# Kernel tuning notes

Measured on AMD Instinct MI355X. Metric: run time of the kernel, lower is better.

Reference implementation:

```python
import jax, jax.numpy as jnp
from jax import lax
import numpy as np

H = 16  # GRU hidden = 4**N_GRAM * 4
V = 4   # 4**N_GRAM
B = 512
S = 8192


def _gru_cell(x, h, Wih, Whh, bih, bhh):
    # PyTorch GRU gate ordering: r, z, n
    gi = x @ Wih.T + bih          # [B, 3H]
    gh = h @ Whh.T + bhh          # [B, 3H]
    ir, iz, inn = jnp.split(gi, 3, axis=-1)
    hr, hz, hn = jnp.split(gh, 3, axis=-1)
    r = jax.nn.sigmoid(ir + hr)
    z = jax.nn.sigmoid(iz + hz)
    n = jnp.tanh(inn + r * hn)
    return (1.0 - z) * n + z * h


def setup_inputs() -> dict:
    key = jax.random.key(0)
    ks = jax.random.split(key, 12)
    f32 = jnp.float32
    k_i = 1.0 / np.sqrt(H)  # torch default GRU/Linear init scale
    u = lambda k, shp: jax.random.uniform(k, shp, f32, -k_i, k_i)
    gt = jax.random.normal(ks[0], (B, V, S), f32)
    return {
        "ground_truth": gt,
        "enc_Wih": u(ks[1], (3 * H, V)),
        "enc_Whh": u(ks[2], (3 * H, H)),
        "enc_bih": u(ks[3], (3 * H,)),
        "enc_bhh": u(ks[4], (3 * H,)),
        "dec_Wih": u(ks[5], (3 * H, V)),
        "dec_Whh": u(ks[6], (3 * H, H)),
        "dec_bih": u(ks[7], (3 * H,)),
        "dec_bhh": u(ks[8], (3 * H,)),
        "out_W": u(ks[9], (V, H)),
        "out_b": u(ks[10], (V,)),
        "emb": jnp.eye(V, dtype=f32),  # one-hot Embedding_LUT (frozen)
        "tf_rate": 1,
    }


def reference(ground_truth, enc_Wih, enc_Whh, enc_bih, enc_bhh,
              dec_Wih, dec_Whh, dec_bih, dec_bhh, out_W, out_b, emb, tf_rate):
    gt = jnp.transpose(ground_truth, (2, 0, 1))      # [S, B, V]
    seq_l, batch, _ = gt.shape
    dt = gt.dtype
    h0 = jnp.zeros((batch, H), dt)

    def enc_step(h, x):
        return _gru_cell(x, h, enc_Wih, enc_Whh, enc_bih, enc_bhh), None
    enc_hidden, _ = lax.scan(enc_step, h0, gt)

    targets = jnp.argmax(gt, axis=2)                 # [S, B] int
    x0 = jnp.zeros((batch, V), dt)
    loss0 = jnp.asarray(0.0, dt)

    if tf_rate >= 1:  # argmax-feedback branch (random() < tf_rate always true)
        def dec_step(carry, tgt):
            x, h, loss = carry
            h = _gru_cell(x, h, dec_Wih, dec_Whh, dec_bih, dec_bhh)
            out = h @ out_W.T + out_b                # [B, V]
            logp = jax.nn.log_softmax(out, axis=-1)
            nll = -jnp.mean(jnp.take_along_axis(logp, tgt[:, None], axis=1))
            top_i = jnp.argmax(out, axis=-1)
            return (emb[top_i], h, loss + nll), None
        (_, _, loss), _ = lax.scan(dec_step, (x0, enc_hidden, loss0), targets)
        output_batch = jnp.zeros((seq_l, batch, V), dt)  # never written in this branch
    else:  # teacher-forcing branch (NLLLoss applied to raw logits, as in source)
        def dec_step(carry, inp):
            x, h, loss = carry
            gt_t, tgt = inp
            h = _gru_cell(x, h, dec_Wih, dec_Whh, dec_bih, dec_bhh)
            out = h @ out_W.T + out_b
            nll = -jnp.mean(jnp.take_along_axis(out, tgt[:, None], axis=1))
            return (gt_t, h, loss + nll), out
        (_, _, loss), output_batch = lax.scan(dec_step, (x0, enc_hidden, loss0), (gt, targets))

    return loss, jnp.transpose(output_batch, (1, 2, 0))  # [B, V, S]
```

## Files before the change

### kernel.cpp

```cpp
#include <hip/hip_runtime.h>

#define S_LEN 8192
#define NH 16
#define NV 4
#define NB 512

typedef _Float16 h2 __attribute__((ext_vector_type(2)));

#define L2E  1.4426950408889634f
#define L2E2 2.8853900817779268f

template<int R>
__device__ __forceinline__ float rotf(float v) {
    return __int_as_float(__builtin_amdgcn_mov_dpp(__float_as_int(v), 0x120 + R, 0xF, 0xF, true));
}
template<int R>
__device__ __forceinline__ h2 roth(h2 v) {
    int i;
    __builtin_memcpy(&i, &v, 4);
    i = __builtin_amdgcn_mov_dpp(i, 0x120 + R, 0xF, 0xF, true);
    h2 o;
    __builtin_memcpy(&o, &i, 4);
    return o;
}
__device__ __forceinline__ float qxor1(float v) {
    return __int_as_float(__builtin_amdgcn_mov_dpp(__float_as_int(v), 0xB1, 0xF, 0xF, true));
}
__device__ __forceinline__ float qxor2(float v) {
    return __int_as_float(__builtin_amdgcn_mov_dpp(__float_as_int(v), 0x4E, 0xF, 0xF, true));
}
__device__ __forceinline__ float qxor3(float v) {
    return __int_as_float(__builtin_amdgcn_mov_dpp(__float_as_int(v), 0x1B, 0xF, 0xF, true));
}

__device__ __forceinline__ float fex2(float x) { return __builtin_amdgcn_exp2f(x); }
__device__ __forceinline__ float frcp(float x) { return __builtin_amdgcn_rcpf(x); }
__device__ __forceinline__ float fsig2(float x) { return frcp(1.0f + fex2(-x)); }
__device__ __forceinline__ float4 ld4(const float* p) { return *(const float4*)p; }

__device__ __forceinline__ h2 pkh(float a, float b) {
    auto t = __builtin_amdgcn_cvt_pkrtz(a, b);
    h2 o;
    __builtin_memcpy(&o, &t, 4);
    return o;
}

__device__ __forceinline__ void bcast32(float v, float& lo, float& hi) {
    lo = v;
    asm("v_permlane32_swap_b32 %0, %1" : "+v"(lo), "+v"(v));
    hi = v;
}

#define FILL_HP16(hp, h)                                      \
    do {                                                      \
        h2 p0_ = pkh((h), rotf<1>(h));                        \
        hp[0] = p0_;                                          \
        hp[1] = roth<2>(p0_);                                 \
        hp[2] = roth<4>(p0_);                                 \
        hp[3] = roth<6>(p0_);                                 \
        hp[4] = roth<8>(p0_);                                 \
        hp[5] = roth<10>(p0_);                                \
        hp[6] = roth<12>(p0_);                                \
        hp[7] = roth<14>(p0_);                                \
    } while (0)

__device__ __forceinline__ float dotd2(const h2* __restrict__ w, const h2* hp, float start) {
    float a = __builtin_amdgcn_fdot2(w[0], hp[0], start, false);
    float b = __builtin_amdgcn_fdot2(w[1], hp[1], 0.0f, false);
    a = __builtin_amdgcn_fdot2(w[2], hp[2], a, false);
    b = __builtin_amdgcn_fdot2(w[3], hp[3], b, false);
    a = __builtin_amdgcn_fdot2(w[4], hp[4], a, false);
    b = __builtin_amdgcn_fdot2(w[5], hp[5], b, false);
    a = __builtin_amdgcn_fdot2(w[6], hp[6], a, false);
    b = __builtin_amdgcn_fdot2(w[7], hp[7], b, false);
    return a + b;
}
__device__ __forceinline__ float dotd2x(const h2* __restrict__ w, const h2* hp, float start) {
    float a = __builtin_amdgcn_fdot2(w[0], hp[0], start, false);
    float b = __builtin_amdgcn_fdot2(w[1], hp[1], 0.0f, false);
    a = __builtin_amdgcn_fdot2(w[2], hp[2], a, false);
    b = __builtin_amdgcn_fdot2(w[3], hp[3], b, false);
    a = __builtin_amdgcn_fdot2(w[4], hp[4], a, false);
    b = __builtin_amdgcn_fdot2(w[5], hp[5], b, false);
    a = __builtin_amdgcn_fdot2(w[6], hp[6], a, false);
    b = __builtin_amdgcn_fdot2(w[7], hp[7], b, false);
    a = __builtin_amdgcn_fdot2(w[8], hp[8], a, false);
    b = __builtin_amdgcn_fdot2(w[9], hp[9], b, false);
    return a + b;
}

__global__ __launch_bounds__(64, 1) void rnn_kernel(
    const float* __restrict__ gt,
    const float* __restrict__ eWih, const float* __restrict__ eWhh,
    const float* __restrict__ ebih, const float* __restrict__ ebhh,
    const float* __restrict__ dWih, const float* __restrict__ dWhh,
    const float* __restrict__ dbih, const float* __restrict__ dbhh,
    const float* __restrict__ oW,  const float* __restrict__ ob,
    float* __restrict__ outs)
{
    const int lane = threadIdx.x;
    const int j    = lane & 15;
    const int q    = j & 3;
    const int row  = lane >> 4;
    const bool isLo = (lane < 32);
    const int b    = blockIdx.x * 2 + (row & 1);

    int probe = __builtin_amdgcn_mov_dpp(j, 0x121, 0xF, 0xF, true);
    const int sgn = (probe == ((j + 1) & 15)) ? 1 : -1;

    float h = 0.0f;

    {
        const float* gb = gt + (size_t)b * (NV * S_LEN);
        const int gA = isLo ? 0 : 1;
        h2 wA[10], wB[10];
#pragma unroll
        for (int p = 0; p < 8; ++p) {
            int k0 = (j + sgn * (2 * p)) & 15;
            int k1 = (j + sgn * (2 * p + 1)) & 15;
            wA[p] = (h2){(_Float16)(L2E * eWhh[(gA * NH + j) * NH + k0]),
                         (_Float16)(L2E * eWhh[(gA * NH + j) * NH + k1])};
            float n0 = isLo ? (L2E2 * eWhh[(2 * NH + j) * NH + k0]) : 0.0f;
            float n1 = isLo ? (L2E2 * eWhh[(2 * NH + j) * NH + k1]) : 0.0f;
            wB[p] = (h2){(_Float16)n0, (_Float16)n1};
        }
#pragma unroll
        for (int p = 0; p < 2; ++p) {
            wA[8 + p] = (h2){(_Float16)(L2E * eWih[(gA * NH + j) * NV + 2 * p]),
                             (_Float16)(L2E * eWih[(gA * NH + j) * NV + 2 * p + 1])};
            float n0 = isLo ? 0.0f : (L2E2 * eWih[(2 * NH + j) * NV + 2 * p]);
            float n1 = isLo ? 0.0f : (L2E2 * eWih[(2 * NH + j) * NV + 2 * p + 1]);
            wB[8 + p] = (h2){(_Float16)n0, (_Float16)n1};
        }
        const float startA = L2E * (ebih[gA * NH + j] + ebhh[gA * NH + j]);
        const float startB = isLo ? (L2E2 * ebhh[2 * NH + j]) : (L2E2 * ebih[2 * NH + j]);

        auto estep = [&](float x0, float x1, float x2, float x3) {
            h2 hp[10];
            FILL_HP16(hp, h);
            hp[8] = pkh(x0, x1);
            hp[9] = pkh(x2, x3);
            float vA = dotd2x(wA, hp, startA);
            float vB = dotd2x(wB, hp, startB);
            float ar, az, hn, inn;
            bcast32(vA, ar, az);
            bcast32(vB, hn, inn);
            float r  = fsig2(ar);
            float z  = fsig2(az);
            float y  = fmaf(r, hn, inn);
            float w2 = fsig2(y);
            float t2 = fmaf(-2.0f, z, 2.0f);
            float tb = fmaf(z, h, z - 1.0f);
            h = fmaf(w2, t2, tb);
        };

        float4 A0 = ld4(gb + 0 * S_LEN), A1 = ld4(gb + 1 * S_LEN),
               A2 = ld4(gb + 2 * S_LEN), A3 = ld4(gb + 3 * S_LEN);
        float4 B0 = ld4(gb + 0 * S_LEN + 4), B1 = ld4(gb + 1 * S_LEN + 4),
               B2 = ld4(gb + 2 * S_LEN + 4), B3 = ld4(gb + 3 * S_LEN + 4);
        for (int t = 0; t < S_LEN; t += 8) {
            estep(A0.x, A1.x, A2.x, A3.x);
            estep(A0.y, A1.y, A2.y, A3.y);
            estep(A0.z, A1.z, A2.z, A3.z);
            estep(A0.w, A1.w, A2.w, A3.w);
            int ta = t + 8;  if (ta > S_LEN - 4) ta = S_LEN - 4;
            A0 = ld4(gb + 0 * S_LEN + ta); A1 = ld4(gb + 1 * S_LEN + ta);
            A2 = ld4(gb + 2 * S_LEN + ta); A3 = ld4(gb + 3 * S_LEN + ta);
            estep(B0.x, B1.x, B2.x, B3.x);
            estep(B0.y, B1.y, B2.y, B3.y);
            estep(B0.z, B1.z, B2.z, B3.z);
            estep(B0.w, B1.w, B2.w, B3.w);
            int tb2 = t + 12; if (tb2 > S_LEN - 4) tb2 = S_LEN - 4;
            B0 = ld4(gb + 0 * S_LEN + tb2); B1 = ld4(gb + 1 * S_LEN + tb2);
            B2 = ld4(gb + 2 * S_LEN + tb2); B3 = ld4(gb + 3 * S_LEN + tb2);
        }
    }

    const int gA = isLo ? 0 : 1;
    h2 wA[8], wB[8];
#pragma unroll
    for (int p = 0; p < 8; ++p) {
        int k0 = (j + sgn * (2 * p)) & 15;
        int k1 = (j + sgn * (2 * p + 1)) & 15;
        wA[p] = (h2){(_Float16)(L2E * dWhh[(gA * NH + j) * NH + k0]),
                     (_Float16)(L2E * dWhh[(gA * NH + j) * NH + k1])};
        float w0 = isLo ? (L2E2 * dWhh[(2 * NH + j) * NH + k0]) : oW[q * NH + k0];
        float w1 = isLo ? (L2E2 * dWhh[(2 * NH + j) * NH + k1]) : oW[q * NH + k1];
        wB[p] = (h2){(_Float16)w0, (_Float16)w1};
    }
    const float bNi  = dbih[2 * NH + j];
    const float bNiS = L2E2 * bNi;
    const float biasA  = L2E * (dbih[gA * NH + j] + dbhh[gA * NH + j]);
    const float startB = isLo ? (L2E2 * dbhh[2 * NH + j]) : ob[q];
    float SA[NV], KN[NV];
#pragma unroll
    for (int m = 0; m < NV; ++m) {
        int c = m ^ q;
        SA[m] = L2E * dWih[(gA * NH + j) * NV + c];
        KN[m] = L2E2 * (bNi + dWih[(2 * NH + j) * NV + c]);
    }

    int oidx = (b << 15) + q;
    const bool storer = isLo && (j < 4);

    auto dstep = [&](int koff) {
        h2 hp[8];
        FILL_HP16(hp, h);
        float aA = dotd2(wA, hp, biasA);
        float vB = dotd2(wB, hp, startB);
        float hn, oa;
        bcast32(vB, hn, oa);
        if (storer) outs[oidx + koff] = oa;
        float ob_ = qxor1(oa);
        float oc_ = qxor2(oa);
        float od_ = qxor3(oa);
        bool cA = ob_ > oa;  float mA = fmaxf(oa, ob_);
        bool cB = od_ > oc_; float mB = fmaxf(oc_, od_);
        bool hi_ = mB > mA;
        float KA  = hi_ ? (cB ? SA[3] : SA[2]) : (cA ? SA[1] : SA[0]);
        float KN_ = hi_ ? (cB ? KN[3] : KN[2]) : (cA ? KN[1] : KN[0]);
        float sg  = fsig2(aA + KA);
        float r, z;
        bcast32(sg, r, z);
        float y   = fmaf(r, hn, KN_);
        float w2  = fsig2(y);
        float t2  = fmaf(-2.0f, z, 2.0f);
        float tb  = fmaf(z, h, z - 1.0f);
        h = fmaf(w2, t2, tb);
    };

    {
        h2 hp[8];
        FILL_HP16(hp, h);
        float aA = dotd2(wA, hp, biasA);
        float vB = dotd2(wB, hp, startB);
        float hn, oa;
        bcast32(vB, hn, oa);
        float sg = fsig2(aA);
        float r, z;
        bcast32(sg, r, z);
        float y  = fmaf(r, hn, bNiS);
        float w2 = fsig2(y);
        float t2 = fmaf(-2.0f, z, 2.0f);
        float tb = fmaf(z, h, z - 1.0f);
        h = fmaf(w2, t2, tb);
    }
    for (int u = 0; u < 8184; u += 8) {
#pragma unroll
        for (int k = 0; k < 8; ++k) dstep(k * 4);
        oidx += 32;
    }
#pragma unroll
    for (int k = 0; k < 7; ++k) dstep(k * 4);
    oidx += 28;

    {
        h2 hp[8];
        FILL_HP16(hp, h);
        float vB = dotd2(wB, hp, startB);
        float hn, oa;
        bcast32(vB, hn, oa);
        if (storer) outs[oidx] = oa;
    }
}

__global__ __launch_bounds__(1024) void loss_kernel(
    const float* __restrict__ gt, float* __restrict__ outs, float* __restrict__ loss)
{
    int tid = blockIdx.x * 1024 + threadIdx.x;
    int t = tid & (S_LEN - 1);
    int b = tid >> 13;
    float4 o = *(const float4*)(outs + (size_t)tid * 4);
    const float* g = gt + (size_t)b * (NV * S_LEN) + t;
    float p0 = g[0], p1 = g[S_LEN], p2 = g[2 * S_LEN], p3 = g[3 * S_LEN];
    int tg = (p1 > p0) ? 1 : 0;  float bm = fmaxf(p0, p1);
    tg = (p2 > bm) ? 2 : tg;     bm = fmaxf(p2, bm);
    tg = (p3 > bm) ? 3 : tg;
    float vt = (tg & 1) ? ((tg & 2) ? o.w : o.y) : ((tg & 2) ? o.z : o.x);
    float mx = fmaxf(fmaxf(o.x, o.y), fmaxf(o.z, o.w));
    float ss = __expf(o.x - mx) + __expf(o.y - mx) + __expf(o.z - mx) + __expf(o.w - mx);
    float v  = (mx - vt) + __logf(ss);
    *(float4*)(outs + (size_t)tid * 4) = make_float4(0.f, 0.f, 0.f, 0.f);
#pragma unroll
    for (int d = 1; d < 64; d <<= 1) v += __shfl_xor(v, d, 64);
    __shared__ float sm[16];
    int w = threadIdx.x >> 6;
    if ((threadIdx.x & 63) == 0) sm[w] = v;
    __syncthreads();
    if (threadIdx.x < 16) {
        float s = sm[threadIdx.x];
#pragma unroll
        for (int d = 1; d < 16; d <<= 1) s += __shfl_xor(s, d, 64);
        if (threadIdx.x == 0) atomicAdd(loss, s * (1.0f / NB));
    }
}

extern "C" void kernel_launch(void* const* d_in, const int* in_sizes, int n_in,
                              void* d_out, int out_size, void* d_ws, size_t ws_size,
                              hipStream_t stream) {
    (void)in_sizes; (void)n_in; (void)d_ws; (void)ws_size; (void)out_size;
    const float* gt   = (const float*)d_in[0];
    const float* eWih = (const float*)d_in[1];
    const float* eWhh = (const float*)d_in[2];
    const float* ebih = (const float*)d_in[3];
    const float* ebhh = (const float*)d_in[4];
    const float* dWih = (const float*)d_in[5];
    const float* dWhh = (const float*)d_in[6];
    const float* dbih = (const float*)d_in[7];
    const float* dbhh = (const float*)d_in[8];
    const float* oW   = (const float*)d_in[9];
    const float* ob   = (const float*)d_in[10];

    float* out  = (float*)d_out;
    float* outs = out + 1;
    (void)hipMemsetAsync(d_out, 0, sizeof(float), stream);
    rnn_kernel<<<NB / 2, 64, 0, stream>>>(gt, eWih, eWhh, ebih, ebhh,
                                          dWih, dWhh, dbih, dbhh, oW, ob, outs);
    loss_kernel<<<(NB * S_LEN) / 1024, 1024, 0, stream>>>(gt, outs, out);
}
```

Baseline: 2.987 ms.

## Assign one batch row per wave, spreading gate rows across 64 lanes

Result: faster. 2.875 ms (median of 2 runs) (-3.7%).

```diff
diff --git a/kernel.cpp b/kernel.cpp
--- a/kernel.cpp
+++ b/kernel.cpp
@@ -49,6 +49,11 @@
     lo = v;
     asm("v_permlane32_swap_b32 %0, %1" : "+v"(lo), "+v"(v));
     hi = v;
+}
+__device__ __forceinline__ void bcast16(float v, float& e, float& o) {
+    e = v;
+    asm("v_permlane16_swap_b32 %0, %1" : "+v"(e), "+v"(v));
+    o = v;
 }
 
 #define FILL_HP16(hp, h)                                      \
@@ -64,29 +69,17 @@
         hp[7] = roth<14>(p0_);                                \
     } while (0)
 
-__device__ __forceinline__ float dotd2(const h2* __restrict__ w, const h2* hp, float start) {
-    float a = __builtin_amdgcn_fdot2(w[0], hp[0], start, false);
-    float b = __builtin_amdgcn_fdot2(w[1], hp[1], 0.0f, false);
-    a = __builtin_amdgcn_fdot2(w[2], hp[2], a, false);
-    b = __builtin_amdgcn_fdot2(w[3], hp[3], b, false);
-    a = __builtin_amdgcn_fdot2(w[4], hp[4], a, false);
-    b = __builtin_amdgcn_fdot2(w[5], hp[5], b, false);
-    a = __builtin_amdgcn_fdot2(w[6], hp[6], a, false);
-    b = __builtin_amdgcn_fdot2(w[7], hp[7], b, false);
-    return a + b;
-}
-__device__ __forceinline__ float dotd2x(const h2* __restrict__ w, const h2* hp, float start) {
-    float a = __builtin_amdgcn_fdot2(w[0], hp[0], start, false);
-    float b = __builtin_amdgcn_fdot2(w[1], hp[1], 0.0f, false);
-    a = __builtin_amdgcn_fdot2(w[2], hp[2], a, false);
-    b = __builtin_amdgcn_fdot2(w[3], hp[3], b, false);
-    a = __builtin_amdgcn_fdot2(w[4], hp[4], a, false);
-    b = __builtin_amdgcn_fdot2(w[5], hp[5], b, false);
-    a = __builtin_amdgcn_fdot2(w[6], hp[6], a, false);
-    b = __builtin_amdgcn_fdot2(w[7], hp[7], b, false);
-    a = __builtin_amdgcn_fdot2(w[8], hp[8], a, false);
-    b = __builtin_amdgcn_fdot2(w[9], hp[9], b, false);
-    return a + b;
+__device__ __forceinline__ float dot8s(const h2* __restrict__ w, const h2* hp, float start) {
+    float a = start;
+#pragma unroll
+    for (int p = 0; p < 8; ++p) a = __builtin_amdgcn_fdot2(w[p], hp[p], a, false);
+    return a;
+}
+__device__ __forceinline__ float dot10s(const h2* __restrict__ w, const h2* hp, float start) {
+    float a = start;
+#pragma unroll
+    for (int p = 0; p < 10; ++p) a = __builtin_amdgcn_fdot2(w[p], hp[p], a, false);
+    return a;
 }
 
 __global__ __launch_bounds__(64, 1) void rnn_kernel(
@@ -102,8 +95,8 @@
     const int j    = lane & 15;
     const int q    = j & 3;
     const int row  = lane >> 4;
-    const bool isLo = (lane < 32);
-    const int b    = blockIdx.x * 2 + (row & 1);
+    const bool loH = (lane < 32);
+    const int b    = blockIdx.x;
 
     int probe = __builtin_amdgcn_mov_dpp(j, 0x121, 0xF, 0xF, true);
     const int sgn = (probe == ((j + 1) & 15)) ? 1 : -1;
@@ -112,42 +105,44 @@
 
     {
         const float* gb = gt + (size_t)b * (NV * S_LEN);
-        const int gA = isLo ? 0 : 1;
-        h2 wA[10], wB[10];
-#pragma unroll
-        for (int p = 0; p < 8; ++p) {
-            int k0 = (j + sgn * (2 * p)) & 15;
-            int k1 = (j + sgn * (2 * p + 1)) & 15;
-            wA[p] = (h2){(_Float16)(L2E * eWhh[(gA * NH + j) * NH + k0]),
-                         (_Float16)(L2E * eWhh[(gA * NH + j) * NH + k1])};
-            float n0 = isLo ? (L2E2 * eWhh[(2 * NH + j) * NH + k0]) : 0.0f;
-            float n1 = isLo ? (L2E2 * eWhh[(2 * NH + j) * NH + k1]) : 0.0f;
-            wB[p] = (h2){(_Float16)n0, (_Float16)n1};
+        h2 w[10];
+        float start;
+        {
+            const int g  = (row == 0) ? 0 : (row == 2) ? 1 : 2;
+            const float schh = (row == 0 || row == 2) ? L2E : (row == 1 ? L2E2 : 0.0f);
+            const float scih = (row == 0 || row == 2) ? L2E : (row == 3 ? L2E2 : 0.0f);
+#pragma unroll
+            for (int p = 0; p < 8; ++p) {
+                int k0 = (j + sgn * (2 * p)) & 15;
+                int k1 = (j + sgn * (2 * p + 1)) & 15;
+                w[p] = (h2){(_Float16)(schh * eWhh[(g * NH + j) * NH + k0]),
+                            (_Float16)(schh * eWhh[(g * NH + j) * NH + k1])};
+            }
+#pragma unroll
+            for (int p = 0; p < 2; ++p) {
+                w[8 + p] = (h2){(_Float16)(scih * eWih[(g * NH + j) * NV + 2 * p]),
+                                (_Float16)(scih * eWih[(g * NH + j) * NV + 2 * p + 1])};
+            }
+            start = (row == 0) ? L2E  * (ebih[j] + ebhh[j])
+                  : (row == 2) ? L2E  * (ebih[NH + j] + ebhh[NH + j])
+                  : (row == 1) ? L2E2 * ebhh[2 * NH + j]
+                               : L2E2 * ebih[2 * NH + j];
         }
-#pragma unroll
-        for (int p = 0; p < 2; ++p) {
-            wA[8 + p] = (h2){(_Float16)(L2E * eWih[(gA * NH + j) * NV + 2 * p]),
-                             (_Float16)(L2E * eWih[(gA * NH + j) * NV + 2 * p + 1])};
-            float n0 = isLo ? 0.0f : (L2E2 * eWih[(2 * NH + j) * NV + 2 * p]);
-            float n1 = isLo ? 0.0f : (L2E2 * eWih[(2 * NH + j) * NV + 2 * p + 1]);
-            wB[8 + p] = (h2){(_Float16)n0, (_Float16)n1};
-        }
-        const float startA = L2E * (ebih[gA * NH + j] + ebhh[gA * NH + j]);
-        const float startB = isLo ? (L2E2 * ebhh[2 * NH + j]) : (L2E2 * ebih[2 * NH + j]);
 
         auto estep = [&](float x0, float x1, float x2, float x3) {
             h2 hp[10];
             FILL_HP16(hp, h);
             hp[8] = pkh(x0, x1);
             hp[9] = pkh(x2, x3);
-            float vA = dotd2x(wA, hp, startA);
-            float vB = dotd2x(wB, hp, startB);
-            float ar, az, hn, inn;
-            bcast32(vA, ar, az);
-            bcast32(vB, hn, inn);
-            float r  = fsig2(ar);
-            float z  = fsig2(az);
-            float y  = fmaf(r, hn, inn);
+            float v = dot10s(w, hp, start);
+            float e, o_;
+            bcast16(v, e, o_);
+            float hn_, inn_;
+            bcast32(o_, hn_, inn_);
+            float sg = fsig2(e);
+            float r, z;
+            bcast32(sg, r, z);
+            float y  = fmaf(r, hn_, inn_);
             float w2 = fsig2(y);
             float t2 = fmaf(-2.0f, z, 2.0f);
             float tb = fmaf(z, h, z - 1.0f);
@@ -176,40 +171,46 @@
         }
     }
 
-    const int gA = isLo ? 0 : 1;
-    h2 wA[8], wB[8];
-#pragma unroll
-    for (int p = 0; p < 8; ++p) {
-        int k0 = (j + sgn * (2 * p)) & 15;
-        int k1 = (j + sgn * (2 * p + 1)) & 15;
-        wA[p] = (h2){(_Float16)(L2E * dWhh[(gA * NH + j) * NH + k0]),
-                     (_Float16)(L2E * dWhh[(gA * NH + j) * NH + k1])};
-        float w0 = isLo ? (L2E2 * dWhh[(2 * NH + j) * NH + k0]) : oW[q * NH + k0];
-        float w1 = isLo ? (L2E2 * dWhh[(2 * NH + j) * NH + k1]) : oW[q * NH + k1];
-        wB[p] = (h2){(_Float16)w0, (_Float16)w1};
+    h2 w[8];
+    float start;
+    {
+        const int g  = (row == 0) ? 0 : (row == 2) ? 1 : 2;
+        const float schh = (row == 0 || row == 2) ? L2E : (row == 1 ? L2E2 : 0.0f);
+#pragma unroll
+        for (int p = 0; p < 8; ++p) {
+            int k0 = (j + sgn * (2 * p)) & 15;
+            int k1 = (j + sgn * (2 * p + 1)) & 15;
+            float w0 = (row == 3) ? oW[q * NH + k0] : schh * dWhh[(g * NH + j) * NH + k0];
+            float w1 = (row == 3) ? oW[q * NH + k1] : schh * dWhh[(g * NH + j) * NH + k1];
+            w[p] = (h2){(_Float16)w0, (_Float16)w1};
+        }
+        start = (row == 0) ? L2E  * (dbih[j] + dbhh[j])
+              : (row == 2) ? L2E  * (dbih[NH + j] + dbhh[NH + j])
+              : (row == 1) ? L2E2 * dbhh[2 * NH + j]
+                           : ob[q];
     }
     const float bNi  = dbih[2 * NH + j];
     const float bNiS = L2E2 * bNi;
-    const float biasA  = L2E * (dbih[gA * NH + j] + dbhh[gA * NH + j]);
-    const float startB = isLo ? (L2E2 * dbhh[2 * NH + j]) : ob[q];
+    const int gS = loH ? 0 : 1;
     float SA[NV], KN[NV];
 #pragma unroll
     for (int m = 0; m < NV; ++m) {
         int c = m ^ q;
-        SA[m] = L2E * dWih[(gA * NH + j) * NV + c];
+        SA[m] = L2E * dWih[(gS * NH + j) * NV + c];
         KN[m] = L2E2 * (bNi + dWih[(2 * NH + j) * NV + c]);
     }
 
     int oidx = (b << 15) + q;
-    const bool storer = isLo && (j < 4);
+    const bool storer = (lane < 4);
 
     auto dstep = [&](int koff) {
         h2 hp[8];
         FILL_HP16(hp, h);
-        float aA = dotd2(wA, hp, biasA);
-        float vB = dotd2(wB, hp, startB);
-        float hn, oa;
-        bcast32(vB, hn, oa);
+        float v = dot8s(w, hp, start);
+        float e, o_;
+        bcast16(v, e, o_);
+        float hn_, oa;
+        bcast32(o_, hn_, oa);
         if (storer) outs[oidx + koff] = oa;
         float ob_ = qxor1(oa);
         float oc_ = qxor2(oa);
@@ -219,10 +220,10 @@
         bool hi_ = mB > mA;
         float KA  = hi_ ? (cB ? SA[3] : SA[2]) : (cA ? SA[1] : SA[0]);
         float KN_ = hi_ ? (cB ? KN[3] : KN[2]) : (cA ? KN[1] : KN[0]);
-        float sg  = fsig2(aA + KA);
+        float sg  = fsig2(e + KA);
         float r, z;
         bcast32(sg, r, z);
-        float y   = fmaf(r, hn, KN_);
+        float y   = fmaf(r, hn_, KN_);
         float w2  = fsig2(y);
         float t2  = fmaf(-2.0f, z, 2.0f);
         float tb  = fmaf(z, h, z - 1.0f);
@@ -232,14 +233,15 @@
     {
         h2 hp[8];
         FILL_HP16(hp, h);
-        float aA = dotd2(wA, hp, biasA);
-        float vB = dotd2(wB, hp, startB);
-        float hn, oa;
-        bcast32(vB, hn, oa);
-        float sg = fsig2(aA);
+        float v = dot8s(w, hp, start);
+        float e, o_;
+        bcast16(v, e, o_);
+        float hn_, oa;
+        bcast32(o_, hn_, oa);
+        float sg = fsig2(e);
         float r, z;
         bcast32(sg, r, z);
-        float y  = fmaf(r, hn, bNiS);
+        float y  = fmaf(r, hn_, bNiS);
         float w2 = fsig2(y);
         float t2 = fmaf(-2.0f, z, 2.0f);
         float tb = fmaf(z, h, z - 1.0f);
@@ -257,9 +259,11 @@
     {
         h2 hp[8];
         FILL_HP16(hp, h);
-        float vB = dotd2(wB, hp, startB);
-        float hn, oa;
-        bcast32(vB, hn, oa);
+        float v = dot8s(w, hp, start);
+        float e, o_;
+        bcast16(v, e, o_);
+        float hn_, oa;
+        bcast32(o_, hn_, oa);
         if (storer) outs[oidx] = oa;
     }
 }
@@ -314,7 +318,7 @@
     float* out  = (float*)d_out;
     float* outs = out + 1;
     (void)hipMemsetAsync(d_out, 0, sizeof(float), stream);
-    rnn_kernel<<<NB / 2, 64, 0, stream>>>(gt, eWih, eWhh, ebih, ebhh,
-                                          dWih, dWhh, dbih, dbhh, oW, ob, outs);
+    rnn_kernel<<<NB, 64, 0, stream>>>(gt, eWih, eWhh, ebih, ebhh,
+                                      dWih, dWhh, dbih, dbhh, oW, ob, outs);
     loss_kernel<<<(NB * S_LEN) / 1024, 1024, 0, stream>>>(gt, outs, out);
 }
```
